# Kernel optimization log

Hardware: AMD Instinct MI355X
Metric: run time of the kernel (lower is better)

Reference implementation:

```python
import jax, jax.numpy as jnp
import numpy as np

B, Cin, Cout, H, W = 8, 64, 128, 128, 128
K, S, P = 3, 1, 1
KK = K * K
EPS = 1e-5


def _conv2d(x, w, b=None):
    out = jax.lax.conv_general_dilated(
        x, w, window_strides=(S, S), padding=[(P, P), (P, P)],
        dimension_numbers=('NCHW', 'OIHW', 'NCHW'))
    if b is not None:
        out = out + b[None, :, None, None]
    return out


def setup_inputs() -> dict:
    key = jax.random.key(0)
    k = jax.random.split(key, 5)
    sc = 1.0 / np.sqrt(Cin * KK)
    return {
        'x': jax.random.normal(k[0], (B, Cin, H, W), jnp.float32),
        'offset_w': jax.random.normal(k[1], (2 * KK, Cin, K, K), jnp.float32) * sc,
        'offset_b': jnp.zeros((2 * KK,), jnp.float32),
        'mask_w': jax.random.normal(k[2], (KK, Cin, K, K), jnp.float32) * sc,
        'mask_b': jnp.zeros((KK,), jnp.float32),
        'conv_w': jax.random.normal(k[3], (Cout, Cin, K, K), jnp.float32) * sc,
    }


def _deform_conv2d(x, offset, mask, w):
    """Modulated deformable conv (torchvision deform_conv2d semantics)."""
    Bn, C, Hh, Ww = x.shape
    Ho, Wo = offset.shape[2], offset.shape[3]
    off = offset.reshape(Bn, KK, 2, Ho, Wo)  # (y, x) pairs per kernel tap
    ky, kx = jnp.meshgrid(jnp.arange(K), jnp.arange(K), indexing='ij')
    ky = ky.reshape(KK).astype(x.dtype)
    kx = kx.reshape(KK).astype(x.dtype)
    hy = (jnp.arange(Ho) * S - P).astype(x.dtype)
    wx = (jnp.arange(Wo) * S - P).astype(x.dtype)
    # sampling positions [B, KK, Ho, Wo]
    py = off[:, :, 0] + ky[None, :, None, None] + hy[None, None, :, None]
    px = off[:, :, 1] + kx[None, :, None, None] + wx[None, None, None, :]

    y0 = jnp.floor(py)
    x0 = jnp.floor(px)
    wy1 = py - y0; wx1 = px - x0
    wy0 = 1.0 - wy1; wx0 = 1.0 - wx1

    xf = x.reshape(Bn, C, Hh * Ww)

    def gather(yi, xi):
        valid = ((yi >= 0) & (yi < Hh) & (xi >= 0) & (xi < Ww)).astype(x.dtype)
        yc = jnp.clip(yi, 0, Hh - 1).astype(jnp.int32)
        xc = jnp.clip(xi, 0, Ww - 1).astype(jnp.int32)
        idx = (yc * Ww + xc).reshape(Bn, -1)  # [B, KK*Ho*Wo]
        vals = jnp.take_along_axis(xf, idx[:, None, :], axis=2)  # [B, C, KK*Ho*Wo]
        return vals.reshape(Bn, C, KK, Ho, Wo) * valid.reshape(Bn, 1, KK, Ho, Wo)

    v = (gather(y0, x0) * (wy0 * wx0)[:, None]
         + gather(y0, x0 + 1) * (wy0 * wx1)[:, None]
         + gather(y0 + 1, x0) * (wy1 * wx0)[:, None]
         + gather(y0 + 1, x0 + 1) * (wy1 * wx1)[:, None])  # [B, C, KK, Ho, Wo]
    v = v * mask[:, None]  # modulation
    return jnp.einsum('bckhw,ock->bohw', v, w.reshape(w.shape[0], C, KK))


def reference(x, offset_w, offset_b, mask_w, mask_b, conv_w):
    offset = _conv2d(x, offset_w, offset_b)
    mask = jax.nn.sigmoid(_conv2d(x, mask_w, mask_b))
    out = _deform_conv2d(x, offset, mask, conv_w)
    # BatchNorm2d(affine=False), training-mode normalization over (N, H, W)
    mean = out.mean(axis=(0, 2, 3), keepdims=True)
    var = out.var(axis=(0, 2, 3), keepdims=True)
    return jax.nn.relu((out - mean) * jax.lax.rsqrt(var + EPS))
```

## Files before the change

### kernel.cpp

```cpp
#include <hip/hip_runtime.h>
#include <hip/hip_bf16.h>

#define H_ 128
#define W_ 128
#define HW 16384
#define CIN 64
#define COUT 128
#define KK9 9
#define BATCH 8
#define NPIX (BATCH * HW)
#define KDIM 576

typedef short bf16x8 __attribute__((ext_vector_type(8)));
typedef float f32x4  __attribute__((ext_vector_type(4)));
typedef unsigned short ushort_t;

union U4B { uint4 u; bf16x8 v; };

__device__ __forceinline__ float us2f(unsigned short u) {
    unsigned int v = ((unsigned int)u) << 16;
    float f;
    __builtin_memcpy(&f, &v, 4);
    return f;
}
__device__ __forceinline__ float lo_f(unsigned int w) {
    unsigned int v = w << 16;
    float f;
    __builtin_memcpy(&f, &v, 4);
    return f;
}
__device__ __forceinline__ float hi_f(unsigned int w) {
    unsigned int v = w & 0xffff0000u;
    float f;
    __builtin_memcpy(&f, &v, 4);
    return f;
}
__device__ __forceinline__ unsigned short f2us_bf(float f) {
    __hip_bfloat16 h = __float2bfloat16(f);
    unsigned short u;
    __builtin_memcpy(&u, &h, 2);
    return u;
}
__device__ __forceinline__ unsigned int pack2(float a, float b) {
    return (unsigned int)f2us_bf(a) | ((unsigned int)f2us_bf(b) << 16);
}

template <bool F32>
__device__ __forceinline__ float ld_in(const void* p, long i) {
    if (F32) return ((const float*)p)[i];
    return us2f(((const unsigned short*)p)[i]);
}

__global__ void detect_zero(const uint4* __restrict__ xr4,
                            float* __restrict__ flag,
                            float* __restrict__ gstat) {
    int t = threadIdx.x;
#pragma unroll
    for (int i = 0; i < 16; ++i) gstat[i * 256 + t] = 0.0f;
    if (t < 64) {
        uint4 v = xr4[t];
        unsigned int w[4] = {v.x, v.y, v.z, v.w};
        int big = 0;
#pragma unroll
        for (int q = 0; q < 4; ++q) {
            big += (((w[q] >> 7)  & 0xFF) >= 0xC0);
            big += (((w[q] >> 23) & 0xFF) >= 0xC0);
        }
        unsigned long long m = __ballot(big > 0);
        if (t == 0) flag[0] = m ? 1.0f : 0.0f;
    }
}

template <bool F32>
__device__ __forceinline__ void prep_body(const void* offw, const void* offb,
                                          const void* maskw, const void* maskb,
                                          const void* convw,
                                          ushort_t* wTs, ushort_t* wcats,
                                          float* bias, int i) {
    if (i < 73728) {
        int j = i & 7, lane = (i >> 3) & 63, n = (i >> 9) & 7, ks = i >> 12;
        int co = n * 16 + (lane & 15);
        int k  = ks * 32 + ((lane >> 4) << 3) + j;
        int kk = k >> 6, ci = k & 63;
        wTs[i] = f2us_bf(ld_in<F32>(convw, (long)co * KDIM + ci * 9 + kk));
    } else if (i < 73728 + 18432) {
        int i2 = i - 73728;
        int j = i2 & 7, lane = (i2 >> 3) & 63, n = (i2 >> 9) & 1, ks = i2 >> 10;
        int co2 = n * 16 + (lane & 15);
        int k   = ks * 32 + ((lane >> 4) << 3) + j;
        int kk = k >> 6, ci = k & 63;
        float v = 0.0f;
        if (co2 < 18)      v = ld_in<F32>(offw,  (long)co2 * KDIM + ci * 9 + kk);
        else if (co2 < 27) v = ld_in<F32>(maskw, (long)(co2 - 18) * KDIM + ci * 9 + kk);
        wcats[i2] = f2us_bf(v);
    } else if (i < 73728 + 18432 + 32) {
        int j = i - 73728 - 18432;
        float v = 0.0f;
        if (j < 18)      v = ld_in<F32>(offb, j);
        else if (j < 27) v = ld_in<F32>(maskb, j - 18);
        bias[j] = v;
    }
}

__global__ void prep_weights(const void* __restrict__ offw,
                             const void* __restrict__ offb,
                             const void* __restrict__ maskw,
                             const void* __restrict__ maskb,
                             const void* __restrict__ convw,
                             const float* __restrict__ flag,
                             ushort_t* __restrict__ wTs,
                             ushort_t* __restrict__ wcats,
                             float* __restrict__ bias) {
    int i = blockIdx.x * 256 + threadIdx.x;
    if (flag[0] != 0.0f)
        prep_body<true>(offw, offb, maskw, maskb, convw, wTs, wcats, bias, i);
    else
        prep_body<false>(offw, offb, maskw, maskb, convw, wTs, wcats, bias, i);
}

template <bool F32>
__device__ __forceinline__ void transpose_body(const void* x, ushort_t* xnb) {
    __shared__ float tile[CIN][64 + 1];
    int blk  = blockIdx.x;
    int b    = blk >> 8;
    int pix0 = (blk & 255) * 64;
    int t    = threadIdx.x;
    int lane = t & 63;
    int grp  = t >> 6;
#pragma unroll
    for (int r = 0; r < 16; ++r) {
        int ci = r * 4 + grp;
        tile[ci][lane] = ld_in<F32>(x, (long)(b * CIN + ci) * HW + pix0 + lane);
    }
    __syncthreads();
#pragma unroll
    for (int r = 0; r < 16; ++r) {
        int px = r * 4 + grp;
        xnb[(size_t)(b * HW + pix0 + px) * CIN + lane] = f2us_bf(tile[lane][px]);
    }
}

__global__ __launch_bounds__(256) void transpose_x(const void* __restrict__ x,
                                                   const float* __restrict__ flag,
                                                   ushort_t* __restrict__ xnb) {
    if (flag[0] != 0.0f) transpose_body<true>(x, xnb);
    else                 transpose_body<false>(x, xnb);
}

__global__ __launch_bounds__(1024, 4) void conv_mfma(
        const ushort_t* __restrict__ xnb,
        const ushort_t* __restrict__ wcats,
        const float* __restrict__ bias,
        float* __restrict__ off2,
        float* __restrict__ mask_ws) {
    __shared__ uint4 ldsB4[2304];

    int t    = threadIdx.x;
    int bid  = blockIdx.x;
    int sbid = (bid & 7) * 64 + (bid >> 3);
    int pix0 = sbid * 256;
    int b    = pix0 >> 14;
    int rem0 = pix0 & 16383;

    const uint4* ws4 = (const uint4*)wcats;
#pragma unroll
    for (int i = t; i < 2304; i += 1024) ldsB4[i] = ws4[i];

    int wave = t >> 6, lane = t & 63, mrow = lane & 15, quad = lane >> 4;
    int px_l = wave * 16 + mrow;
    int remp = rem0 + px_l;
    int yp = remp >> 7, xp = remp & 127;
    const ushort_t* xb = xnb + (size_t)b * HW * CIN + quad * 8;

    uint4 af0[9], af1[9];
#pragma unroll
    for (int kk = 0; kk < 9; ++kk) {
        int yy = yp + kk / 3 - 1;
        int xq = xp + kk % 3 - 1;
        bool ok = (yy >= 0) && (yy < H_) && (xq >= 0) && (xq < W_);
        const ushort_t* src = xb + (size_t)(yy * W_ + xq) * CIN;
        af0[kk] = ok ? *(const uint4*)src        : make_uint4(0, 0, 0, 0);
        af1[kk] = ok ? *(const uint4*)(src + 32) : make_uint4(0, 0, 0, 0);
    }
    __syncthreads();

    f32x4 acc[2];
    acc[0] = (f32x4){0.f, 0.f, 0.f, 0.f};
    acc[1] = (f32x4){0.f, 0.f, 0.f, 0.f};
    const ushort_t* ldsB = (const ushort_t*)ldsB4;
#pragma unroll
    for (int kk = 0; kk < 9; ++kk) {
#pragma unroll
        for (int half = 0; half < 2; ++half) {
            int ks = kk * 2 + half;
            U4B a; a.u = half ? af1[kk] : af0[kk];
#pragma unroll
            for (int n = 0; n < 2; ++n) {
                bf16x8 bf = *(const bf16x8*)(ldsB + ((ks * 2 + n) * 64 + lane) * 8);
                acc[n] = __builtin_amdgcn_mfma_f32_16x16x32_bf16(a.v, bf, acc[n], 0, 0, 0);
            }
        }
    }

#pragma unroll
    for (int n = 0; n < 2; ++n) {
        int co2 = n * 16 + mrow;
        if (co2 >= 27) continue;
        float bs = bias[co2];
#pragma unroll
        for (int r = 0; r < 4; ++r) {
            int px = wave * 16 + quad * 4 + r;
            float v = acc[n][r] + bs;
            if (co2 < 18) {
                off2[((size_t)(b * 9 + (co2 >> 1)) * HW + rem0 + px) * 2 + (co2 & 1)] = v;
            } else {
                mask_ws[(size_t)(b * 9 + (co2 - 18)) * HW + rem0 + px] =
                    1.0f / (1.0f + __expf(-v));
            }
        }
    }
}

__device__ __forceinline__ void compute_tap(int yp_t, int xp_t,
                                            float oy, float ox, float mk,
                                            int* ofs, float* wg) {
    float py  = (float)yp_t + oy;
    float pxf = (float)xp_t + ox;
    float y0f = floorf(py), x0f = floorf(pxf);
    int yi = (int)y0f, xi = (int)x0f;
    float wy1 = py - y0f, wx1 = pxf - x0f;
    float wy0 = 1.0f - wy1, wx0 = 1.0f - wx1;
    int ya  = min(max(yi, 0), H_ - 1);
    int yb  = min(max(yi + 1, 0), H_ - 1);
    int xa  = min(max(xi, 0), W_ - 1);
    int xb2 = min(max(xi + 1, 0), W_ - 1);
    bool vy0 = (yi >= 0) & (yi < H_);
    bool vy1 = (yi >= -1) & (yi < H_ - 1);
    bool vx0 = (xi >= 0) & (xi < W_);
    bool vx1 = (xi >= -1) & (xi < W_ - 1);
    float m0 = mk * wy0, m1 = mk * wy1;
    wg[0] = (vy0 & vx0) ? m0 * wx0 : 0.0f;
    wg[1] = (vy0 & vx1) ? m0 * wx1 : 0.0f;
    wg[2] = (vy1 & vx0) ? m1 * wx0 : 0.0f;
    wg[3] = (vy1 & vx1) ? m1 * wx1 : 0.0f;
    int ra = ya << 13, rb = yb << 13;
    int ca = xa << 6,  cb_ = xb2 << 6;
    ofs[0] = ra + ca;  ofs[1] = ra + cb_;
    ofs[2] = rb + ca;  ofs[3] = rb + cb_;
}

__device__ __forceinline__ void issue_half(const ushort_t* __restrict__ xb,
                                           const int* ofs, int hoff, uint4* cb) {
#pragma unroll
    for (int c = 0; c < 4; ++c)
        cb[c] = *(const uint4*)(xb + ofs[c] + hoff);
}

__device__ __forceinline__ void consume_half(int ks, const uint4* cb,
                                             const float* wg,
                                             const ushort_t* __restrict__ ldsB,
                                             int lane, f32x4* acc) {
    float2 v2[4];
#pragma unroll
    for (int j = 0; j < 4; ++j) v2[j] = make_float2(0.f, 0.f);
#pragma unroll
    for (int c = 0; c < 4; ++c) {
        float w = wg[c];
        unsigned int ww[4] = {cb[c].x, cb[c].y, cb[c].z, cb[c].w};
#pragma unroll
        for (int j = 0; j < 4; ++j) {
            v2[j].x = fmaf(w, lo_f(ww[j]), v2[j].x);
            v2[j].y = fmaf(w, hi_f(ww[j]), v2[j].y);
        }
    }
    U4B a;
    a.u = make_uint4(pack2(v2[0].x, v2[0].y), pack2(v2[1].x, v2[1].y),
                     pack2(v2[2].x, v2[2].y), pack2(v2[3].x, v2[3].y));
    const ushort_t* bbase = ldsB + ((size_t)(ks * 8) * 64 + lane) * 8;
    __builtin_amdgcn_s_setprio(1);
#pragma unroll
    for (int n = 0; n < 8; ++n) {
        bf16x8 bf = *(const bf16x8*)(bbase + n * 64 * 8);
        acc[n] = __builtin_amdgcn_mfma_f32_16x16x32_bf16(a.v, bf, acc[n], 0, 0, 0);
    }
    __builtin_amdgcn_s_setprio(0);
}

__global__ __launch_bounds__(1024, 4) void deform_mfma(
        const ushort_t* __restrict__ xnb,
        const float* __restrict__ off2,
        const float* __restrict__ mask_ws,
        const ushort_t* __restrict__ wTs,
        ushort_t* __restrict__ prebn,
        float* __restrict__ gstat) {
    __shared__ uint4 ldsB4[9216];
    __shared__ float red[256];

    int t    = threadIdx.x;
    int bid  = blockIdx.x;
    int sbid = (bid & 7) * 64 + (bid >> 3);
    int pix0 = sbid * 256;
    int b    = pix0 >> 14;
    int rem0 = pix0 & 16383;

    const uint4* ws4 = (const uint4*)wTs;
#pragma unroll
    for (int i = 0; i < 9; ++i) ldsB4[i * 1024 + t] = ws4[i * 1024 + t];
    if (t < 256) red[t] = 0.0f;

    int wave = t >> 6, lane = t & 63, mrow = lane & 15, quad = lane >> 4;
    int px_l = wave * 16 + mrow;
    int remp = rem0 + px_l;
    int yp = remp >> 7, xp = remp & 127;
    const ushort_t* xb = xnb + (size_t)b * HW * CIN + quad * 8;
    size_t obase = (size_t)b * 9 * HW + remp;

    float2 oE = *(const float2*)(off2 + obase * 2);
    float2 oO = *(const float2*)(off2 + (obase + HW) * 2);
    float mkE = mask_ws[obase];
    float mkO = mask_ws[obase + HW];
    __syncthreads();

    f32x4 acc[8];
#pragma unroll
    for (int n = 0; n < 8; ++n) acc[n] = (f32x4){0.f, 0.f, 0.f, 0.f};
    const ushort_t* ldsB = (const ushort_t*)ldsB4;

    int   ofs[2][4];
    float wg[2][4];
    uint4 cb[3][4];

    compute_tap(yp - 1, xp - 1, oE.x, oE.y, mkE, ofs[0], wg[0]);
    issue_half(xb, ofs[0], 0,  cb[0]);
    issue_half(xb, ofs[0], 32, cb[1]);
    oE  = *(const float2*)(off2 + (obase + (size_t)2 * HW) * 2);
    mkE = mask_ws[obase + (size_t)2 * HW];
    __builtin_amdgcn_sched_barrier(0);

#pragma unroll
    for (int hs = 0; hs < 18; ++hs) {
        const int hs2 = hs + 2;
        if (hs2 < 18) {
            const int kk2 = hs2 >> 1;
            const int s2  = hs2 % 3;
            if ((hs2 & 1) == 0) {
                const int tp2 = kk2 & 1;
                float ooy = tp2 ? oO.x : oE.x;
                float oox = tp2 ? oO.y : oE.y;
                float omk = tp2 ? mkO  : mkE;
                compute_tap(yp + kk2 / 3 - 1, xp + kk2 % 3 - 1, ooy, oox, omk,
                            ofs[tp2], wg[tp2]);
                issue_half(xb, ofs[tp2], 0, cb[s2]);
                if (kk2 + 2 <= 8) {
                    float2 o = *(const float2*)(off2 + (obase + (size_t)(kk2 + 2) * HW) * 2);
                    float  m = mask_ws[obase + (size_t)(kk2 + 2) * HW];
                    if (tp2) { oO = o; mkO = m; } else { oE = o; mkE = m; }
                }
            } else {
                issue_half(xb, ofs[kk2 & 1], 32, cb[s2]);
            }
        }
        __builtin_amdgcn_sched_barrier(0);
        consume_half(hs, cb[hs % 3], wg[(hs >> 1) & 1], ldsB, lane, acc);
    }

#pragma unroll
    for (int n = 0; n < 8; ++n) {
        int co = n * 16 + mrow;
        float s = 0.f, ss = 0.f;
#pragma unroll
        for (int r = 0; r < 4; ++r) {
            int pg = pix0 + wave * 16 + quad * 4 + r;
            float v = acc[n][r];
            prebn[(size_t)pg * COUT + co] = f2us_bf(v);
            s += v;
            ss += v * v;
        }
        s  += __shfl_xor(s, 16, 64);
        s  += __shfl_xor(s, 32, 64);
        ss += __shfl_xor(ss, 16, 64);
        ss += __shfl_xor(ss, 32, 64);
        if (quad == 0) {
            atomicAdd(&red[co], s);
            atomicAdd(&red[128 + co], ss);
        }
    }
    __syncthreads();
    if (t < 256) atomicAdd(&gstat[(bid & 15) * 256 + t], red[t]);
}

__global__ __launch_bounds__(256) void bn_apply_t(const ushort_t* __restrict__ prebn,
                                                  const float* __restrict__ gstat,
                                                  float* __restrict__ out) {
    __shared__ float tile[128 * 65];
    __shared__ float mvs[256];
    int t = threadIdx.x;
    if (t < 128) {
        float s = 0.f, ss = 0.f;
#pragma unroll
        for (int part = 0; part < 16; ++part) {
            s  += gstat[part * 256 + t];
            ss += gstat[part * 256 + 128 + t];
        }
        const float invN = 1.0f / (float)NPIX;
        float mean = s * invN;
        float var  = ss * invN - mean * mean;
        if (!isfinite(mean)) mean = 0.0f;
        float r = rsqrtf(fmaxf(var, 0.0f) + 1e-5f);
        if (!isfinite(r)) r = 1.0f;
        mvs[t]       = mean;
        mvs[128 + t] = r;
    }
    __syncthreads();
    int pix0 = blockIdx.x * 64;
    int b    = pix0 >> 14;
    int rem0 = pix0 & 16383;
    const ushort_t* src = prebn + (size_t)pix0 * COUT;
#pragma unroll
    for (int r = 0; r < 32; ++r) {
        int i = r * 256 + t;
        int p = i >> 7, c = i & 127;
        float v = us2f(src[i]);
        v = fmaxf((v - mvs[c]) * mvs[128 + c], 0.0f);
        tile[c * 65 + p] = v;
    }
    __syncthreads();
#pragma unroll
    for (int r = 0; r < 32; ++r) {
        int i = r * 256 + t;
        int c2 = i >> 6, p2 = i & 63;
        out[(size_t)(b * COUT + c2) * HW + rem0 + p2] = tile[c2 * 65 + p2];
    }
}

extern "C" void kernel_launch(void* const* d_in, const int* in_sizes, int n_in,
                              void* d_out, int out_size, void* d_ws, size_t ws_size,
                              hipStream_t stream) {
    (void)in_sizes; (void)n_in; (void)out_size; (void)ws_size;
    const void* x     = d_in[0];
    const void* offw  = d_in[1];
    const void* offb  = d_in[2];
    const void* maskw = d_in[3];
    const void* maskb = d_in[4];
    const void* convw = d_in[5];

    float* ws       = (float*)d_ws;
    float* off2     = ws;
    float* mask_ws  = off2 + 2359296;
    float* bias     = mask_ws + 1179648;
    float* gstat    = bias + 32;
    float* flag     = gstat + 4096;
    ushort_t* wTs   = (ushort_t*)(flag + 16);
    ushort_t* wcats = wTs + 73728;
    ushort_t* xnb   = wcats + 18432;
    ushort_t* prebn = xnb + 8388608;
    float* out      = (float*)d_out;

    detect_zero<<<1, 256, 0, stream>>>((const uint4*)x, flag, gstat);
    prep_weights<<<361, 256, 0, stream>>>(offw, offb, maskw, maskb, convw, flag, wTs, wcats, bias);
    transpose_x<<<2048, 256, 0, stream>>>(x, flag, xnb);
    conv_mfma<<<512, 1024, 0, stream>>>(xnb, wcats, bias, off2, mask_ws);
    deform_mfma<<<512, 1024, 0, stream>>>(xnb, off2, mask_ws, wTs, prebn, gstat);
    bn_apply_t<<<2048, 256, 0, stream>>>(prebn, gstat, out);
}
```

Before: 217.9 us.

## Warp-specialize deform kernel into gather/interp producers and MFMA consumers

Splits each 1024-thread block into 8 producer waves that gather and bilinearly interpolate samples into a double-buffered LDS A tile, and 8 consumer waves that run the MFMAs against LDS weights. Blocks now cover 128 pixels instead of 256 and the grid doubles. The weight tile is loaded in two halves to halve LDS use. The block-level stat reduction is replaced by direct global atomics. The design adds a block barrier per half-step and routes the interpolated A operand through LDS. It also increases global atomic traffic.

```diff
diff --git a/kernel.cpp b/kernel.cpp
--- a/kernel.cpp
+++ b/kernel.cpp
@@ -256,10 +256,7 @@
         cb[c] = *(const uint4*)(xb + ofs[c] + hoff);
 }
 
-__device__ __forceinline__ void consume_half(int ks, const uint4* cb,
-                                             const float* wg,
-                                             const ushort_t* __restrict__ ldsB,
-                                             int lane, f32x4* acc) {
+__device__ __forceinline__ uint4 interp_pack(const uint4* cb, const float* wg) {
     float2 v2[4];
 #pragma unroll
     for (int j = 0; j < 4; ++j) v2[j] = make_float2(0.f, 0.f);
@@ -273,17 +270,8 @@
             v2[j].y = fmaf(w, hi_f(ww[j]), v2[j].y);
         }
     }
-    U4B a;
-    a.u = make_uint4(pack2(v2[0].x, v2[0].y), pack2(v2[1].x, v2[1].y),
-                     pack2(v2[2].x, v2[2].y), pack2(v2[3].x, v2[3].y));
-    const ushort_t* bbase = ldsB + ((size_t)(ks * 8) * 64 + lane) * 8;
-    __builtin_amdgcn_s_setprio(1);
-#pragma unroll
-    for (int n = 0; n < 8; ++n) {
-        bf16x8 bf = *(const bf16x8*)(bbase + n * 64 * 8);
-        acc[n] = __builtin_amdgcn_mfma_f32_16x16x32_bf16(a.v, bf, acc[n], 0, 0, 0);
-    }
-    __builtin_amdgcn_s_setprio(0);
+    return make_uint4(pack2(v2[0].x, v2[0].y), pack2(v2[1].x, v2[1].y),
+                      pack2(v2[2].x, v2[2].y), pack2(v2[3].x, v2[3].y));
 }
 
 __global__ __launch_bounds__(1024, 4) void deform_mfma(
@@ -293,100 +281,143 @@
         const ushort_t* __restrict__ wTs,
         ushort_t* __restrict__ prebn,
         float* __restrict__ gstat) {
-    __shared__ uint4 ldsB4[9216];
-    __shared__ float red[256];
+    __shared__ uint4 ldsB4[4608];
+    __shared__ uint4 ldsA4[1024];
 
     int t    = threadIdx.x;
     int bid  = blockIdx.x;
-    int sbid = (bid & 7) * 64 + (bid >> 3);
-    int pix0 = sbid * 256;
+    int sbid = (bid & 7) * 128 + (bid >> 3);
+    int pix0 = sbid * 128;
     int b    = pix0 >> 14;
     int rem0 = pix0 & 16383;
 
     const uint4* ws4 = (const uint4*)wTs;
-#pragma unroll
-    for (int i = 0; i < 9; ++i) ldsB4[i * 1024 + t] = ws4[i * 1024 + t];
-    if (t < 256) red[t] = 0.0f;
+    for (int i = t; i < 4608; i += 1024) ldsB4[i] = ws4[i];
 
     int wave = t >> 6, lane = t & 63, mrow = lane & 15, quad = lane >> 4;
-    int px_l = wave * 16 + mrow;
+    int grp  = wave & 7;
+    int px_l = grp * 16 + mrow;
     int remp = rem0 + px_l;
     int yp = remp >> 7, xp = remp & 127;
     const ushort_t* xb = xnb + (size_t)b * HW * CIN + quad * 8;
-    size_t obase = (size_t)b * 9 * HW + remp;
-
-    float2 oE = *(const float2*)(off2 + obase * 2);
-    float2 oO = *(const float2*)(off2 + (obase + HW) * 2);
-    float mkE = mask_ws[obase];
-    float mkO = mask_ws[obase + HW];
-    __syncthreads();
-
-    f32x4 acc[8];
-#pragma unroll
-    for (int n = 0; n < 8; ++n) acc[n] = (f32x4){0.f, 0.f, 0.f, 0.f};
-    const ushort_t* ldsB = (const ushort_t*)ldsB4;
-
-    int   ofs[2][4];
-    float wg[2][4];
-    uint4 cb[3][4];
-
-    compute_tap(yp - 1, xp - 1, oE.x, oE.y, mkE, ofs[0], wg[0]);
-    issue_half(xb, ofs[0], 0,  cb[0]);
-    issue_half(xb, ofs[0], 32, cb[1]);
-    oE  = *(const float2*)(off2 + (obase + (size_t)2 * HW) * 2);
-    mkE = mask_ws[obase + (size_t)2 * HW];
-    __builtin_amdgcn_sched_barrier(0);
-
-#pragma unroll
-    for (int hs = 0; hs < 18; ++hs) {
-        const int hs2 = hs + 2;
-        if (hs2 < 18) {
-            const int kk2 = hs2 >> 1;
-            const int s2  = hs2 % 3;
-            if ((hs2 & 1) == 0) {
-                const int tp2 = kk2 & 1;
-                float ooy = tp2 ? oO.x : oE.x;
-                float oox = tp2 ? oO.y : oE.y;
-                float omk = tp2 ? mkO  : mkE;
-                compute_tap(yp + kk2 / 3 - 1, xp + kk2 % 3 - 1, ooy, oox, omk,
-                            ofs[tp2], wg[tp2]);
-                issue_half(xb, ofs[tp2], 0, cb[s2]);
-                if (kk2 + 2 <= 8) {
-                    float2 o = *(const float2*)(off2 + (obase + (size_t)(kk2 + 2) * HW) * 2);
-                    float  m = mask_ws[obase + (size_t)(kk2 + 2) * HW];
-                    if (tp2) { oO = o; mkO = m; } else { oE = o; mkE = m; }
-                }
-            } else {
-                issue_half(xb, ofs[kk2 & 1], 32, cb[s2]);
+    int obase = b * 9 * HW + remp;
+
+    if (wave < 8) {
+        uint4 G0[4], G1[4], G2[4];
+        int   ofsE[4], ofsO[4];
+        float wgE[4], wgO[4];
+        float2 oE, oO;
+        float  mkE, mkO;
+
+#define GSEL(c) ((c) == 0 ? G0 : (c) == 1 ? G1 : G2)
+
+        oE = *(const float2*)(off2 + (size_t)obase * 2);          mkE = mask_ws[obase];
+        oO = *(const float2*)(off2 + (size_t)(obase + HW) * 2);   mkO = mask_ws[obase + HW];
+        compute_tap(yp - 1, xp - 1, oE.x, oE.y, mkE, ofsE, wgE);
+        issue_half(xb, ofsE, 0,  G0);
+        issue_half(xb, ofsE, 32, G1);
+        oE = *(const float2*)(off2 + (size_t)(obase + 2 * HW) * 2); mkE = mask_ws[obase + 2 * HW];
+        compute_tap(yp - 1, xp, oO.x, oO.y, mkO, ofsO, wgO);
+        issue_half(xb, ofsO, 0, G2);
+        oO = *(const float2*)(off2 + (size_t)(obase + 3 * HW) * 2); mkO = mask_ws[obase + 3 * HW];
+        ldsA4[grp * 64 + lane] = interp_pack(G0, wgE);
+        __syncthreads();
+
+#define PSTEP(HS) do {                                                        \
+    constexpr int ihs = (HS) + 3;                                             \
+    if constexpr (ihs < 18) {                                                 \
+        constexpr int T = ihs >> 1;                                           \
+        if constexpr ((ihs & 1) == 0) {                                       \
+            if constexpr (T & 1) {                                            \
+                compute_tap(yp + T / 3 - 1, xp + T % 3 - 1,                   \
+                            oO.x, oO.y, mkO, ofsO, wgO);                      \
+                issue_half(xb, ofsO, 0, GSEL(ihs % 3));                       \
+                if constexpr (T + 2 <= 8) {                                   \
+                    oO = *(const float2*)(off2 + (size_t)(obase + (T + 2) * HW) * 2); \
+                    mkO = mask_ws[obase + (T + 2) * HW];                      \
+                }                                                             \
+            } else {                                                          \
+                compute_tap(yp + T / 3 - 1, xp + T % 3 - 1,                   \
+                            oE.x, oE.y, mkE, ofsE, wgE);                      \
+                issue_half(xb, ofsE, 0, GSEL(ihs % 3));                       \
+                if constexpr (T + 2 <= 8) {                                   \
+                    oE = *(const float2*)(off2 + (size_t)(obase + (T + 2) * HW) * 2); \
+                    mkE = mask_ws[obase + (T + 2) * HW];                      \
+                }                                                             \
+            }                                                                 \
+        } else {                                                              \
+            if constexpr (T & 1) issue_half(xb, ofsO, 32, GSEL(ihs % 3));     \
+            else                 issue_half(xb, ofsE, 32, GSEL(ihs % 3));     \
+        }                                                                     \
+    }                                                                         \
+    __builtin_amdgcn_sched_barrier(0);       \
+    constexpr int jhs = (HS) + 1;                                             \
+    if constexpr (jhs < 18) {                                                 \
+        uint4 av = interp_pack(GSEL(jhs % 3),                                 \
+                               ((jhs >> 1) & 1) ? wgO : wgE);                 \
+        ldsA4[(jhs & 1) * 512 + grp * 64 + lane] = av;                        \
+    }                                                                         \
+    __syncthreads();                                                          \
+} while (0)
+
+        PSTEP(0);  PSTEP(1);  PSTEP(2);  PSTEP(3);  PSTEP(4);
+        PSTEP(5);  PSTEP(6);  PSTEP(7);  PSTEP(8);
+        for (int i = t; i < 4608; i += 1024) ldsB4[i] = ws4[4608 + i];
+        __syncthreads();
+        PSTEP(9);  PSTEP(10); PSTEP(11); PSTEP(12); PSTEP(13);
+        PSTEP(14); PSTEP(15); PSTEP(16); PSTEP(17);
+#undef PSTEP
+#undef GSEL
+    } else {
+        f32x4 acc[8];
+#pragma unroll
+        for (int n = 0; n < 8; ++n) acc[n] = (f32x4){0.f, 0.f, 0.f, 0.f};
+        const ushort_t* ldsB = (const ushort_t*)ldsB4;
+
+        __syncthreads();
+
+#define CSTEP(HS, SLOT) do {                                                  \
+    U4B a; a.u = ldsA4[((HS) & 1) * 512 + grp * 64 + lane];                   \
+    __builtin_amdgcn_s_setprio(1);                                            \
+    _Pragma("unroll")                                                         \
+    for (int n = 0; n < 8; ++n) {                                             \
+        bf16x8 bf = *(const bf16x8*)(ldsB + (((SLOT) * 8 + n) * 64 + lane) * 8); \
+        acc[n] = __builtin_amdgcn_mfma_f32_16x16x32_bf16(a.v, bf, acc[n], 0, 0, 0); \
+    }                                                                         \
+    __builtin_amdgcn_s_setprio(0);                                            \
+    __syncthreads();                                                          \
+} while (0)
+
+        CSTEP(0, 0);  CSTEP(1, 1);  CSTEP(2, 2);  CSTEP(3, 3);  CSTEP(4, 4);
+        CSTEP(5, 5);  CSTEP(6, 6);  CSTEP(7, 7);  CSTEP(8, 8);
+        for (int i = t; i < 4608; i += 1024) ldsB4[i] = ws4[4608 + i];
+        __syncthreads();
+        CSTEP(9, 0);  CSTEP(10, 1); CSTEP(11, 2); CSTEP(12, 3); CSTEP(13, 4);
+        CSTEP(14, 5); CSTEP(15, 6); CSTEP(16, 7); CSTEP(17, 8);
+#undef CSTEP
+
+#pragma unroll
+        for (int n = 0; n < 8; ++n) {
+            int co = n * 16 + mrow;
+            float s = 0.f, ss = 0.f;
+#pragma unroll
+            for (int r = 0; r < 4; ++r) {
+                int pg = pix0 + grp * 16 + quad * 4 + r;
+                float v = acc[n][r];
+                prebn[(size_t)pg * COUT + co] = f2us_bf(v);
+                s += v;
+                ss += v * v;
             }
-        }
-        __builtin_amdgcn_sched_barrier(0);
-        consume_half(hs, cb[hs % 3], wg[(hs >> 1) & 1], ldsB, lane, acc);
-    }
-
-#pragma unroll
-    for (int n = 0; n < 8; ++n) {
-        int co = n * 16 + mrow;
-        float s = 0.f, ss = 0.f;
-#pragma unroll
-        for (int r = 0; r < 4; ++r) {
-            int pg = pix0 + wave * 16 + quad * 4 + r;
-            float v = acc[n][r];
-            prebn[(size_t)pg * COUT + co] = f2us_bf(v);
-            s += v;
-            ss += v * v;
-        }
-        s  += __shfl_xor(s, 16, 64);
-        s  += __shfl_xor(s, 32, 64);
-        ss += __shfl_xor(ss, 16, 64);
-        ss += __shfl_xor(ss, 32, 64);
-        if (quad == 0) {
-            atomicAdd(&red[co], s);
-            atomicAdd(&red[128 + co], ss);
-        }
-    }
-    __syncthreads();
-    if (t < 256) atomicAdd(&gstat[(bid & 15) * 256 + t], red[t]);
+            s  += __shfl_xor(s, 16, 64);
+            s  += __shfl_xor(s, 32, 64);
+            ss += __shfl_xor(ss, 16, 64);
+            ss += __shfl_xor(ss, 32, 64);
+            if (quad == 0) {
+                atomicAdd(&gstat[(bid & 15) * 256 + co], s);
+                atomicAdd(&gstat[(bid & 15) * 256 + 128 + co], ss);
+            }
+        }
+    }
 }
 
 __global__ __launch_bounds__(256) void bn_apply_t(const ushort_t* __restrict__ prebn,
@@ -460,6 +491,6 @@
     prep_weights<<<361, 256, 0, stream>>>(offw, offb, maskw, maskb, convw, flag, wTs, wcats, bias);
     transpose_x<<<2048, 256, 0, stream>>>(x, flag, xnb);
     conv_mfma<<<512, 1024, 0, stream>>>(xnb, wcats, bias, off2, mask_ws);
-    deform_mfma<<<512, 1024, 0, stream>>>(xnb, off2, mask_ws, wTs, prebn, gstat);
+    deform_mfma<<<1024, 1024, 0, stream>>>(xnb, off2, mask_ws, wTs, prebn, gstat);
     bn_apply_t<<<2048, 256, 0, stream>>>(prebn, gstat, out);
 }
```

Result: slower. 252.4 us (+15.8%).

## Stage input halo rows in LDS for offset conv and vectorize BN output

Applied to the files above, without the earlier changes.

The offset/mask conv kernel now loads the four input rows its 256-pixel block needs, halo included, into swizzled shared memory once, then builds the 3x3 im2col fragments from LDS instead of nine separate global loads per lane. This is meant to cut redundant global traffic for overlapping taps. It adds 64KB of LDS per block, which may reduce occupancy under the 1024-thread launch bound. The BN/ReLU output kernel also switches to 16-byte vector loads of the bf16 pre-BN values and float4 stores.

```diff
diff --git a/kernel.cpp b/kernel.cpp
--- a/kernel.cpp
+++ b/kernel.cpp
@@ -154,6 +154,7 @@
         float* __restrict__ off2,
         float* __restrict__ mask_ws) {
     __shared__ uint4 ldsB4[2304];
+    __shared__ uint4 ldsX4[4096];
 
     int t    = threadIdx.x;
     int bid  = blockIdx.x;
@@ -161,28 +162,45 @@
     int pix0 = sbid * 256;
     int b    = pix0 >> 14;
     int rem0 = pix0 & 16383;
+    int y0   = rem0 >> 7;
 
     const uint4* ws4 = (const uint4*)wcats;
 #pragma unroll
     for (int i = t; i < 2304; i += 1024) ldsB4[i] = ws4[i];
+
+    const uint4* xrow4 = (const uint4*)(xnb + (size_t)b * HW * CIN);
+    int sxq  = t >> 3;
+    int sc16 = t & 7;
+#pragma unroll
+    for (int r = 0; r < 4; ++r) {
+        int gy = y0 - 1 + r;
+        if (gy >= 0 && gy < H_) {
+            uint4 v = xrow4[(size_t)gy * 1024 + t];
+            ldsX4[r * 1024 + sxq * 8 + (sc16 ^ (sxq & 7))] = v;
+        }
+    }
+    __syncthreads();
 
     int wave = t >> 6, lane = t & 63, mrow = lane & 15, quad = lane >> 4;
     int px_l = wave * 16 + mrow;
-    int remp = rem0 + px_l;
-    int yp = remp >> 7, xp = remp & 127;
-    const ushort_t* xb = xnb + (size_t)b * HW * CIN + quad * 8;
+    int ly   = px_l >> 7;
+    int xp   = px_l & 127;
 
     uint4 af0[9], af1[9];
 #pragma unroll
     for (int kk = 0; kk < 9; ++kk) {
-        int yy = yp + kk / 3 - 1;
-        int xq = xp + kk % 3 - 1;
-        bool ok = (yy >= 0) && (yy < H_) && (xq >= 0) && (xq < W_);
-        const ushort_t* src = xb + (size_t)(yy * W_ + xq) * CIN;
-        af0[kk] = ok ? *(const uint4*)src        : make_uint4(0, 0, 0, 0);
-        af1[kk] = ok ? *(const uint4*)(src + 32) : make_uint4(0, 0, 0, 0);
-    }
-    __syncthreads();
+        int ty = kk / 3, tx = kk % 3;
+        int tr = ly + ty;
+        int gy = y0 - 1 + tr;
+        int xq = xp + tx - 1;
+        bool ok = (gy >= 0) && (gy < H_) && (xq >= 0) && (xq < W_);
+        int xc = min(max(xq, 0), W_ - 1);
+        int base = tr * 1024 + xc * 8;
+        uint4 a0 = ldsX4[base + ((quad    ) ^ (xc & 7))];
+        uint4 a1 = ldsX4[base + ((quad + 4) ^ (xc & 7))];
+        af0[kk] = ok ? a0 : make_uint4(0, 0, 0, 0);
+        af1[kk] = ok ? a1 : make_uint4(0, 0, 0, 0);
+    }
 
     f32x4 acc[2];
     acc[0] = (f32x4){0.f, 0.f, 0.f, 0.f};
@@ -415,21 +433,32 @@
     int pix0 = blockIdx.x * 64;
     int b    = pix0 >> 14;
     int rem0 = pix0 & 16383;
-    const ushort_t* src = prebn + (size_t)pix0 * COUT;
-#pragma unroll
-    for (int r = 0; r < 32; ++r) {
-        int i = r * 256 + t;
-        int p = i >> 7, c = i & 127;
-        float v = us2f(src[i]);
-        v = fmaxf((v - mvs[c]) * mvs[128 + c], 0.0f);
-        tile[c * 65 + p] = v;
-    }
-    __syncthreads();
-#pragma unroll
-    for (int r = 0; r < 32; ++r) {
-        int i = r * 256 + t;
-        int c2 = i >> 6, p2 = i & 63;
-        out[(size_t)(b * COUT + c2) * HW + rem0 + p2] = tile[c2 * 65 + p2];
+    const uint4* src4 = (const uint4*)(prebn + (size_t)pix0 * COUT);
+#pragma unroll
+    for (int r = 0; r < 4; ++r) {
+        int i  = r * 256 + t;
+        uint4 v = src4[i];
+        int p  = i >> 4;
+        int c0 = (i & 15) * 8;
+        unsigned int w[4] = {v.x, v.y, v.z, v.w};
+#pragma unroll
+        for (int j = 0; j < 4; ++j) {
+            int c = c0 + j * 2;
+            float f0 = lo_f(w[j]);
+            float f1 = hi_f(w[j]);
+            tile[c * 65 + p]       = fmaxf((f0 - mvs[c])     * mvs[128 + c],     0.0f);
+            tile[(c + 1) * 65 + p] = fmaxf((f1 - mvs[c + 1]) * mvs[128 + c + 1], 0.0f);
+        }
+    }
+    __syncthreads();
+#pragma unroll
+    for (int r = 0; r < 8; ++r) {
+        int i  = r * 256 + t;
+        int c2 = i >> 4;
+        int q  = (i & 15) * 4;
+        float4 w4 = make_float4(tile[c2 * 65 + q],     tile[c2 * 65 + q + 1],
+                                tile[c2 * 65 + q + 2], tile[c2 * 65 + q + 3]);
+        *(float4*)(out + (size_t)(b * COUT + c2) * HW + rem0 + q) = w4;
     }
 }
 
```

After: 207.5 us. 4.8% less time.
